# Optimization experiments

Measured on AMD Instinct MI355X. Metric: run time of the kernel, lower is better.

The kernel has to match this reference:

```python
import jax, jax.numpy as jnp
import numpy as np

IN_SHAPE, OUT_SHAPE = 64, 256  # FoldingBlock(64, 256, ...)
REPEAT = OUT_SHAPE // IN_SHAPE  # 4


def sample_2d(m, n):
    # Reproduces SANet.points + SANet.sample_2D exactly (numpy constants).
    xs = np.linspace(-0.3, 0.3, 46)
    ys = np.linspace(-0.3, 0.3, 46)
    X, Y = np.meshgrid(xs, ys)            # (46,46) each, 'xy' indexing
    pts = np.stack([X, Y])                # (2,46,46)
    ix = np.round(np.linspace(0, 45, m)).astype(int)
    iy = np.round(np.linspace(0, 45, n)).astype(int)
    gx, gy = np.meshgrid(ix, iy)          # (n,m)
    p = pts[:, gx.ravel(), gy.ravel()].T  # (m*n, 2)
    return jnp.asarray(p, dtype=jnp.float32)


def _lin_relu(x, W, b):
    return jax.nn.relu(x @ W + b)


def setup_inputs() -> dict:
    key = jax.random.key(0)
    ks = jax.random.split(key, 16)
    s = 0.02  # small init scale keeps softmax logits well-conditioned
    d = {
        "p": jax.random.normal(ks[0], (128, 64, 512), dtype=jnp.float32),
        # upmlp1: MLP([514, 512]) (shared by both up() calls)
        "W_up": jax.random.normal(ks[1], (514, 512), dtype=jnp.float32) * s,
        "b_up": jnp.zeros((512,), jnp.float32),
        # self_attn1: M_h = MLP([1024,256])
        "Wh": jax.random.normal(ks[2], (1024, 256), dtype=jnp.float32) * s,
        "bh": jnp.zeros((256,), jnp.float32),
        # M_l = MLP([1024,256])
        "Wl": jax.random.normal(ks[3], (1024, 256), dtype=jnp.float32) * s,
        "bl": jnp.zeros((256,), jnp.float32),
        # M_g = MLP([1024,1024])
        "Wg": jax.random.normal(ks[4], (1024, 1024), dtype=jnp.float32) * s,
        "bg": jnp.zeros((1024,), jnp.float32),
        # M_f = MLP([1024,512,256]) -> two Linear+ReLU layers
        "Wf1": jax.random.normal(ks[5], (1024, 512), dtype=jnp.float32) * s,
        "bf1": jnp.zeros((512,), jnp.float32),
        "Wf2": jax.random.normal(ks[6], (512, 256), dtype=jnp.float32) * s,
        "bf2": jnp.zeros((256,), jnp.float32),
        # M_down: MLP([1024, 512])
        "W_down": jax.random.normal(ks[7], (1024, 512), dtype=jnp.float32) * s,
        "b_down": jnp.zeros((512,), jnp.float32),
        "m": 16,
        "n": 16,
    }
    return d


def _up(p, pts, W_up, b_up, Wh, bh, Wl, bl, Wg, bg, Wf1, bf1, Wf2, bf2):
    # p: (B, 64, 512) -> (B, 256, 512) via torch-style repeat (tile)
    B = p.shape[0]
    p = jnp.tile(p, (1, REPEAT, 1))
    p2d = jnp.concatenate([p, jnp.broadcast_to(pts[None], (B,) + pts.shape)], -1)  # (B,256,514)
    p2d = _lin_relu(p2d, W_up, b_up)                  # (B,256,512)
    p = jnp.concatenate([p, p2d], -1)                  # (B,256,1024)
    # SelfAttention (hand-rolled: separate projections + softmax + bmm)
    h = _lin_relu(p, Wh, bh)                           # (B,256,256)
    l = _lin_relu(p, Wl, bl)                           # (B,256,256)
    g = _lin_relu(p, Wg, bg)                           # (B,256,1024)
    mm = jnp.einsum("bmc,bnc->bmn", l, h)             # l @ h^T
    attn = jax.nn.softmax(mm, axis=-1)
    applied = jnp.einsum("bmn,bnc->bmc", attn, g)      # (B,256,1024)
    x = p + applied
    # M_f = MLP([1024,512,256]): ReLU after every Linear
    return _lin_relu(_lin_relu(x, Wf1, bf1), Wf2, bf2)  # (B,256,256)


def _down(p, W_down, b_down):
    # (B,256,256) -> (B,64,1024) -> MLP([1024,512])
    B = p.shape[0]
    p = p.reshape(B, IN_SHAPE, REPEAT * p.shape[2])
    return _lin_relu(p, W_down, b_down)                # (B,64,512)


def reference(p, W_up, b_up, Wh, bh, Wl, bl, Wg, bg, Wf1, bf1, Wf2, bf2,
              W_down, b_down, m, n):
    pts = sample_2d(int(m), int(n))                    # (m*n, 2) constant grid
    attn_params = (Wh, bh, Wl, bl, Wg, bg, Wf1, bf1, Wf2, bf2)
    p1 = _up(p, pts, W_up, b_up, *attn_params)         # (B,256,256)
    p2 = _down(p1, W_down, b_down)                     # (B,64,512)
    p_delta = p - p2
    p2u = _up(p_delta, pts, W_up, b_up, *attn_params)  # shared weights with first up
    return p1 + p2u                                    # (B,256,256)
```

## Files before the change

### kernel.cpp

```cpp
#include <hip/hip_runtime.h>
#include <cstdint>
#include <cstddef>


typedef unsigned short u16;
typedef __bf16 bf16x8 __attribute__((ext_vector_type(8)));
typedef float f32x4 __attribute__((ext_vector_type(4)));

__device__ __forceinline__ u16 f2bf(float f) {
    unsigned u = __builtin_bit_cast(unsigned, f);
    unsigned r = (u + 0x7fffu + ((u >> 16) & 1u)) >> 16;
    return (u16)r;
}
__device__ __forceinline__ float bf2f(u16 h) {
    unsigned u = ((unsigned)h) << 16;
    return __builtin_bit_cast(float, u);
}
__device__ __forceinline__ void gload16(const u16* g, u16* l) {
    __builtin_amdgcn_global_load_lds((__attribute__((address_space(1))) void*)g,
                                     (__attribute__((address_space(3))) void*)l,
                                     16, 0, 0);
}
__device__ __forceinline__ unsigned ldsaddr(const u16* p) {
    return (unsigned)(size_t)(const __attribute__((address_space(3))) u16*)p;
}
__device__ __forceinline__ bf16x8 dsr128(unsigned a) {
    f32x4 r;
    asm volatile("ds_read_b128 %0, %1" : "=v"(r) : "v"(a));
    return __builtin_bit_cast(bf16x8, r);
}

#define FENCE asm volatile("" ::: "memory")
#define BAR() do { FENCE; __builtin_amdgcn_s_barrier(); FENCE; } while (0)
#define VMC(N) asm volatile("s_waitcnt vmcnt(" #N ")" ::: "memory")
#define LGKM(N) do { asm volatile("s_waitcnt lgkmcnt(" #N ")" ::: "memory"); \
                     __builtin_amdgcn_sched_barrier(0); } while (0)

template<int MODE>
__global__ __launch_bounds__(512, 1)
void bp(const u16* __restrict__ A0, const u16* __restrict__ A1,
        const u16* __restrict__ Bt, const float* __restrict__ bias,
        const float* __restrict__ EXf, const u16* __restrict__ EXb,
        u16* __restrict__ outB, u16* __restrict__ out1, u16* __restrict__ out2,
        int K, long sB)
{
    __shared__ __align__(16) u16 As[2][16384];
    __shared__ __align__(16) u16 Bs[2][16384];

    const int b    = blockIdx.y;
    const int tid  = threadIdx.x;
    const int lane = tid & 63;
    const int w    = tid >> 6;
    const int wr   = w >> 2, wc = w & 3;
    const int wrow0 = wr * 128, wcol0 = wc * 64;
    const int gn0  = blockIdx.x * 256;
    const int lm   = lane & 15, hk = lane >> 4;
    const int NT   = K / 64;

    const int srow = tid & 255;
    const int su   = tid >> 8;

    const u16* gA0;
    const u16* gA1 = nullptr;
    if constexpr (MODE == 0) {
        gA0 = A0 + ((size_t)b << 15) + (size_t)(srow & 63) * 512 + su * 8;
    } else if constexpr (MODE == 1) {
        gA0 = A0 + ((size_t)b << 15) + (size_t)(srow & 63) * 512 + su * 8;
        gA1 = A1 + ((size_t)b << 17) + (size_t)srow * 512 + su * 8;
    } else if constexpr (MODE == 3) {
        gA0 = A0 + ((size_t)b << 16) + (size_t)srow * 256 + su * 8;
    } else {
        gA0 = A0 + ((size_t)b << 18) + (size_t)srow * 1024 + su * 8;
    }
    const u16* gB0 = Bt + (size_t)b * sB + (size_t)(gn0 + srow) * K + su * 8;

    u16* dA = &As[0][(size_t)(su * 256 + srow) * 8];
    u16* dB = &Bs[0][(size_t)(su * 256 + srow) * 8];

    auto stgA = [&](int kt, int buf, int rp) {
        const u16* g;
        if constexpr (MODE == 1) g = (kt < 8) ? (gA0 + kt * 64) : (gA1 + (kt - 8) * 64);
        else                     g = gA0 + kt * 64;
        u16* d = dA + buf * 16384 + rp * 8192;
        gload16(g + rp * 32,      d);
        gload16(g + rp * 32 + 16, d + 4096);
    };
    auto stgB = [&](int kt, int buf, int rp) {
        const u16* g = gB0 + kt * 64 + rp * 32;
        u16* d = dB + buf * 16384 + rp * 8192;
        gload16(g,      d);
        gload16(g + 16, d + 4096);
    };

    const unsigned aBase = ldsaddr(&As[0][0]) + (unsigned)(hk * 256 + wrow0 + lm) * 16u;
    const unsigned bBase = ldsaddr(&Bs[0][0]) + (unsigned)(hk * 256 + wcol0 + lm) * 16u;

    f32x4 acc[8][4];
    #pragma unroll
    for (int i = 0; i < 8; ++i)
        #pragma unroll
        for (int j = 0; j < 4; ++j)
            acc[i][j] = (f32x4){0.f, 0.f, 0.f, 0.f};

#define MFMA_Q(IB) do { \
    _Pragma("unroll") for (int i_ = 0; i_ < 4; ++i_) \
        _Pragma("unroll") for (int j_ = 0; j_ < 4; ++j_) \
            acc[(IB) + i_][j_] = __builtin_amdgcn_mfma_f32_16x16x32_bf16( \
                aq[i_], bq[j_], acc[(IB) + i_][j_], 0, 0, 0); \
} while (0)

    stgA(0, 0, 0); stgA(0, 0, 1);
    stgB(0, 0, 0); stgB(0, 0, 1);
    stgA(1, 1, 0); stgB(1, 1, 0);
    VMC(4);
    BAR();

    for (int t = 0; t < NT; ++t) {
        const int buf = t & 1, nx = buf ^ 1;
        const unsigned ab = aBase + (unsigned)buf * 32768u;
        const unsigned bb = bBase + (unsigned)buf * 32768u;
        bf16x8 aq[4], bq[4];

        #pragma unroll
        for (int i = 0; i < 4; ++i) aq[i] = dsr128(ab + (unsigned)(i * 256));
        #pragma unroll
        for (int j = 0; j < 4; ++j) bq[j] = dsr128(bb + (unsigned)(j * 256));
        if (t + 1 < NT) stgA(t + 1, nx, 1);
        BAR();
        LGKM(0);
        __builtin_amdgcn_s_setprio(1);
        MFMA_Q(0);
        __builtin_amdgcn_s_setprio(0);
        BAR();

        #pragma unroll
        for (int i = 0; i < 4; ++i) aq[i] = dsr128(ab + (unsigned)(1024 + i * 256));
        if (t + 1 < NT) stgB(t + 1, nx, 1);
        BAR();
        LGKM(0);
        __builtin_amdgcn_s_setprio(1);
        MFMA_Q(4);
        __builtin_amdgcn_s_setprio(0);
        BAR();

        #pragma unroll
        for (int i = 0; i < 4; ++i) aq[i] = dsr128(ab + (unsigned)(16384 + i * 256));
        #pragma unroll
        for (int j = 0; j < 4; ++j) bq[j] = dsr128(bb + (unsigned)(16384 + j * 256));
        if (t + 2 < NT) stgA(t + 2, buf, 0);
        BAR();
        LGKM(0);
        __builtin_amdgcn_s_setprio(1);
        MFMA_Q(0);
        __builtin_amdgcn_s_setprio(0);
        BAR();

        #pragma unroll
        for (int i = 0; i < 4; ++i) aq[i] = dsr128(ab + (unsigned)(17408 + i * 256));
        if (t + 2 < NT) stgB(t + 2, buf, 0);
        if (t + 2 < NT) { VMC(4); } else { VMC(0); }
        BAR();
        LGKM(0);
        __builtin_amdgcn_s_setprio(1);
        MFMA_Q(4);
        __builtin_amdgcn_s_setprio(0);
        BAR();
    }
#undef MFMA_Q

    #pragma unroll
    for (int i = 0; i < 8; ++i) {
        const int rowb = wrow0 + i * 16 + hk * 4;
        #pragma unroll
        for (int j = 0; j < 4; ++j) {
            const int col = gn0 + wcol0 + j * 16 + lm;
            float v4[4];
            #pragma unroll
            for (int r = 0; r < 4; ++r) v4[r] = acc[i][j][r];

            if constexpr (MODE == 0) {
                #pragma unroll
                for (int r = 0; r < 4; ++r) {
                    const int row = rowb + r;
                    float v = v4[r];
                    const float px = -0.3f + 0.04f * (float)(row >> 4);
                    const float py = -0.3f + 0.04f * (float)(row & 15);
                    v += px * EXf[(size_t)512 * 512 + col] + py * EXf[(size_t)513 * 512 + col];
                    v = fmaxf(v + bias[col], 0.0f);
                    outB[((size_t)b << 17) + (size_t)row * 512 + col] = f2bf(v);
                }
            } else if constexpr (MODE == 1) {
                if (col < 512) {
                    #pragma unroll
                    for (int r = 0; r < 4; ++r) {
                        const int row = rowb + r;
                        float v = fmaxf(v4[r] + bias[col], 0.0f);
                        if (col < 256) outB[((size_t)b << 16) + (size_t)row * 256 + col] = f2bf(v);
                        else           out1[((size_t)b << 16) + (size_t)row * 256 + (col - 256)] = f2bf(v);
                    }
                } else {
                    ushort4 o;
                    o.x = f2bf(fmaxf(v4[0] + bias[col], 0.0f));
                    o.y = f2bf(fmaxf(v4[1] + bias[col], 0.0f));
                    o.z = f2bf(fmaxf(v4[2] + bias[col], 0.0f));
                    o.w = f2bf(fmaxf(v4[3] + bias[col], 0.0f));
                    *reinterpret_cast<ushort4*>(out2 + ((size_t)b << 18) +
                        (size_t)(col - 512) * 256 + rowb) = o;
                }
            } else if constexpr (MODE == 3) {
                #pragma unroll
                for (int r = 0; r < 4; ++r) {
                    const int row = rowb + r;
                    float v = v4[r];
                    float cv;
                    if (col < 512) {
                        const size_t ridx = ((size_t)b << 15) + (size_t)(row & 63) * 512 + col;
                        cv = EXf ? EXf[ridx] : bf2f(EXb[ridx]);
                    } else {
                        cv = bf2f(A1[((size_t)b << 17) + (size_t)row * 512 + (col - 512)]);
                    }
                    v += cv;
                    outB[((size_t)b << 18) + (size_t)row * 1024 + col] = f2bf(v);
                }
            } else {
                #pragma unroll
                for (int r = 0; r < 4; ++r) {
                    const int row = rowb + r;
                    float v = fmaxf(v4[r] + bias[col], 0.0f);
                    outB[((size_t)b << 17) + (size_t)row * 512 + col] = f2bf(v);
                }
            }
        }
    }
}

template<int MODE>
__global__ __launch_bounds__(256, 2)
void mg(const u16* __restrict__ A0, const u16* __restrict__ Bt,
        const float* __restrict__ bias, const float* __restrict__ EXf,
        float* __restrict__ outF, u16* __restrict__ outB,
        int K, long sB)
{
    __shared__ __align__(16) u16 As[2][128 * 64];
    __shared__ __align__(16) u16 Bs[2][128 * 64];

    const int b    = blockIdx.z;
    const int tid  = threadIdx.x;
    const int lane = tid & 63;
    const int w    = tid >> 6;
    const int wr   = w >> 1, wc = w & 1;
    const int wrow0 = wr * 64, wcol0 = wc * 64;
    const int gm0  = blockIdx.y * 128;
    const int gn0  = blockIdx.x * 128;
    const int lm   = lane & 15, hk = lane >> 4;
    const int NT = K / 64;

    auto stage = [&](int kt, int buf) {
        const int kb = kt * 64;
        #pragma unroll
        for (int tp = 0; tp < 4; ++tp) {
            const int idx = tid + tp * 256;
            const int U = idx >> 7, row = idx & 127;
            const int kk = kb + U * 8;
            const u16* ga;
            if constexpr (MODE == 2) {
                ga = A0 + ((size_t)b << 16) + (size_t)(gm0 + row) * 256 + kk;
            } else if constexpr (MODE == 5) {
                ga = A0 + ((size_t)b << 17) + (size_t)(gm0 + row) * 512 + kk;
            } else {
                int gr = gm0 + row; if (gr > 63) gr = 63;
                ga = A0 + ((size_t)b << 16) + (size_t)(gr * 4 + (kk >> 8)) * 256 + (kk & 255);
            }
            gload16(ga, &As[buf][(size_t)idx * 8]);
        }
        #pragma unroll
        for (int tp = 0; tp < 4; ++tp) {
            const int idx = tid + tp * 256;
            const int U = idx >> 7, row = idx & 127;
            const int kk = kb + U * 8;
            gload16(Bt + (size_t)b * sB + (size_t)(gn0 + row) * K + kk,
                    &Bs[buf][(size_t)idx * 8]);
        }
    };

    const unsigned aBase = ldsaddr(&As[0][0]) + (unsigned)(hk * 128 + wrow0 + lm) * 16u;
    const unsigned bBase = ldsaddr(&Bs[0][0]) + (unsigned)(hk * 128 + wcol0 + lm) * 16u;

    f32x4 acc[4][4];
    #pragma unroll
    for (int i = 0; i < 4; ++i)
        #pragma unroll
        for (int j = 0; j < 4; ++j)
            acc[i][j] = (f32x4){0.f, 0.f, 0.f, 0.f};

    stage(0, 0);
    if (NT > 1) stage(1, 1);

    for (int kt = 0; kt < NT; ++kt) {
        const int cur = kt & 1;
        if (kt == NT - 1) { VMC(0); } else { VMC(8); }
        __builtin_amdgcn_s_barrier();
        FENCE;
        const unsigned ab = aBase + (unsigned)cur * 16384u;
        const unsigned bb = bBase + (unsigned)cur * 16384u;
        bf16x8 a0[4], b0[4], a1[4], b1[4];
        #pragma unroll
        for (int i = 0; i < 4; ++i) a0[i] = dsr128(ab + (unsigned)(i * 256));
        #pragma unroll
        for (int j = 0; j < 4; ++j) b0[j] = dsr128(bb + (unsigned)(j * 256));
        #pragma unroll
        for (int i = 0; i < 4; ++i) a1[i] = dsr128(ab + (unsigned)(8192 + i * 256));
        #pragma unroll
        for (int j = 0; j < 4; ++j) b1[j] = dsr128(bb + (unsigned)(8192 + j * 256));
        LGKM(8);
        __builtin_amdgcn_s_setprio(1);
        #pragma unroll
        for (int i = 0; i < 4; ++i)
            #pragma unroll
            for (int j = 0; j < 4; ++j)
                acc[i][j] = __builtin_amdgcn_mfma_f32_16x16x32_bf16(a0[i], b0[j], acc[i][j], 0, 0, 0);
        __builtin_amdgcn_s_setprio(0);
        LGKM(0);
        __builtin_amdgcn_s_setprio(1);
        #pragma unroll
        for (int i = 0; i < 4; ++i)
            #pragma unroll
            for (int j = 0; j < 4; ++j)
                acc[i][j] = __builtin_amdgcn_mfma_f32_16x16x32_bf16(a1[i], b1[j], acc[i][j], 0, 0, 0);
        __builtin_amdgcn_s_setprio(0);
        FENCE;
        __builtin_amdgcn_s_barrier();
        if (kt + 2 < NT) stage(kt + 2, cur);
    }

    #pragma unroll
    for (int i = 0; i < 4; ++i) {
        #pragma unroll
        for (int r = 0; r < 4; ++r) {
            const int row = gm0 + wrow0 + i * 16 + hk * 4 + r;
            if (MODE == 6 && row >= 64) continue;
            #pragma unroll
            for (int j = 0; j < 4; ++j) {
                const int col = gn0 + wcol0 + j * 16 + lm;
                float v = acc[i][j][r];
                if constexpr (MODE == 2) {
                    outF[((size_t)b << 16) + (size_t)row * 256 + col] = v;
                } else if constexpr (MODE == 5) {
                    v = fmaxf(v + bias[col], 0.0f);
                    const size_t oidx = ((size_t)b << 16) + (size_t)row * 256 + col;
                    if (EXf) v += EXf[oidx];
                    outF[oidx] = v;
                    if (outB) outB[oidx] = f2bf(v);
                } else {
                    v = fmaxf(v + bias[col], 0.0f);
                    const size_t oidx = ((size_t)b << 15) + (size_t)row * 512 + col;
                    v = EXf[oidx] - v;
                    outB[oidx] = f2bf(v);
                }
            }
        }
    }
}

template<bool F32IN>
__global__ __launch_bounds__(256)
void transpose_k(const void* __restrict__ in_, u16* __restrict__ out, int R, int C)
{
    __shared__ float t[64][65];
    const size_t zo = (size_t)blockIdx.z * (size_t)R * C;
    const int c0 = blockIdx.x * 64, r0 = blockIdx.y * 64;
    const int x = threadIdx.x, y = threadIdx.y;
    #pragma unroll
    for (int i = 0; i < 16; ++i) {
        const int r = y * 16 + i;
        float v;
        if constexpr (F32IN) v = ((const float*)in_)[zo + (size_t)(r0 + r) * C + c0 + x];
        else                 v = bf2f(((const u16*)in_)[zo + (size_t)(r0 + r) * C + c0 + x]);
        t[r][x] = v;
    }
    __syncthreads();
    #pragma unroll
    for (int i = 0; i < 16; ++i) {
        const int c = y * 16 + i;
        out[zo + (size_t)(c0 + c) * R + r0 + x] = f2bf(t[x][c]);
    }
}

__global__ __launch_bounds__(256)
void cvt_k(const float* __restrict__ in, u16* __restrict__ out, int n4)
{
    int i = blockIdx.x * 256 + threadIdx.x;
    const int stride = gridDim.x * 256;
    for (; i < n4; i += stride) {
        float4 v = ((const float4*)in)[i];
        ushort4 o;
        o.x = f2bf(v.x); o.y = f2bf(v.y); o.z = f2bf(v.z); o.w = f2bf(v.w);
        ((ushort4*)out)[i] = o;
    }
}

__global__ __launch_bounds__(512)
void concat3_k(const float* __restrict__ a, const float* __restrict__ bb,
               const float* __restrict__ c, float* __restrict__ o)
{
    const int i = blockIdx.x * 512 + threadIdx.x;
    if (i < 256)       o[i] = a[i];
    else if (i < 512)  o[i] = bb[i - 256];
    else if (i < 1536) o[i] = c[i - 512];
}

__global__ __launch_bounds__(64)
void softmax_k(const float* __restrict__ logits, u16* __restrict__ attn)
{
    const size_t row = blockIdx.x;
    const float4 v = ((const float4*)(logits + row * 256))[threadIdx.x];
    float mx = fmaxf(fmaxf(v.x, v.y), fmaxf(v.z, v.w));
    #pragma unroll
    for (int o = 32; o > 0; o >>= 1) mx = fmaxf(mx, __shfl_xor(mx, o));
    float e0 = expf(v.x - mx), e1 = expf(v.y - mx), e2 = expf(v.z - mx), e3 = expf(v.w - mx);
    float s = e0 + e1 + e2 + e3;
    #pragma unroll
    for (int o = 32; o > 0; o >>= 1) s += __shfl_xor(s, o);
    const float inv = 1.0f / s;
    ushort4 o;
    o.x = f2bf(e0 * inv); o.y = f2bf(e1 * inv); o.z = f2bf(e2 * inv); o.w = f2bf(e3 * inv);
    ((ushort4*)(attn + row * 256))[threadIdx.x] = o;
}

extern "C" void kernel_launch(void* const* d_in, const int* in_sizes, int n_in,
                              void* d_out, int out_size, void* d_ws, size_t ws_size,
                              hipStream_t stream)
{
    const float* p      = (const float*)d_in[0];
    const float* W_up   = (const float*)d_in[1];
    const float* b_up   = (const float*)d_in[2];
    const float* Wh     = (const float*)d_in[3];
    const float* bh     = (const float*)d_in[4];
    const float* Wl     = (const float*)d_in[5];
    const float* bl     = (const float*)d_in[6];
    const float* Wg     = (const float*)d_in[7];
    const float* bg_    = (const float*)d_in[8];
    const float* Wf1    = (const float*)d_in[9];
    const float* bf1    = (const float*)d_in[10];
    const float* Wf2    = (const float*)d_in[11];
    const float* bf2v   = (const float*)d_in[12];
    const float* W_down = (const float*)d_in[13];
    const float* b_down = (const float*)d_in[14];

    const int B = in_sizes[0] / 32768;
    float* out = (float*)d_out;

    char* wsp = (char*)d_ws;
    auto alloc = [&](size_t bytes) -> char* {
        char* r = wsp; wsp += (bytes + 255) & ~(size_t)255; return r;
    };

    u16* WupT  = (u16*)alloc((size_t)512 * 512 * 2);
    u16* WhlgT = (u16*)alloc((size_t)1536 * 1024 * 2);
    u16* Wf1T  = (u16*)alloc((size_t)512 * 1024 * 2);
    u16* Wf2T  = (u16*)alloc((size_t)256 * 512 * 2);
    u16* WdT   = (u16*)alloc((size_t)512 * 1024 * 2);
    float* bias_hlg = (float*)alloc((size_t)1536 * 4);
    u16* pbf   = (u16*)alloc((size_t)B * 32768 * 2);

    const size_t fixed_used = (size_t)(wsp - (char*)d_ws);
    const size_t perB = 1903104;
    int BC = B;
    while (BC > 1 && fixed_used + (size_t)BC * perB + 4096 > ws_size) BC >>= 1;

    u16* upout = (u16*)alloc((size_t)BC * 131072 * 2);
    u16* gT    = (u16*)alloc((size_t)BC * 262144 * 2);
    u16* xb    = (u16*)alloc((size_t)BC * 262144 * 2);
    u16* hb    = (u16*)alloc((size_t)BC * 65536 * 2);
    u16* lb    = (u16*)alloc((size_t)BC * 65536 * 2);
    u16* atb   = (u16*)alloc((size_t)BC * 65536 * 2);
    u16* p1bf  = (u16*)alloc((size_t)BC * 65536 * 2);
    u16* pdbf  = (u16*)alloc((size_t)BC * 32768 * 2);
    float* lgt = (float*)xb;

    const dim3 tb(64, 4);
    {
        int n4 = B * 8192;
        int nb = (n4 + 255) / 256; if (nb > 2048) nb = 2048;
        cvt_k<<<dim3(nb), dim3(256), 0, stream>>>(p, pbf, n4);
        transpose_k<true><<<dim3(8, 8, 1),  tb, 0, stream>>>(W_up, WupT, 512, 512);
        transpose_k<true><<<dim3(4, 16, 1), tb, 0, stream>>>(Wh, WhlgT, 1024, 256);
        transpose_k<true><<<dim3(4, 16, 1), tb, 0, stream>>>(Wl, WhlgT + (size_t)256 * 1024, 1024, 256);
        transpose_k<true><<<dim3(16, 16, 1),tb, 0, stream>>>(Wg, WhlgT + (size_t)512 * 1024, 1024, 1024);
        transpose_k<true><<<dim3(8, 16, 1), tb, 0, stream>>>(Wf1, Wf1T, 1024, 512);
        transpose_k<true><<<dim3(4, 8, 1),  tb, 0, stream>>>(Wf2, Wf2T, 512, 256);
        transpose_k<true><<<dim3(8, 16, 1), tb, 0, stream>>>(W_down, WdT, 1024, 512);
        concat3_k<<<dim3(3), dim3(512), 0, stream>>>(bh, bl, bg_, bias_hlg);
    }

    auto run_up = [&](const u16* pin_bf, const float* pin_f32, const u16* pin_ebf,
                      float* f2outF, u16* f2outB, const float* f2EXf, int bc) {
        bp<0><<<dim3(2, bc), dim3(512), 0, stream>>>(
            pin_bf, nullptr, WupT, b_up, W_up, nullptr, upout, nullptr, nullptr, 512, 0);
        bp<1><<<dim3(6, bc), dim3(512), 0, stream>>>(
            pin_bf, upout, WhlgT, bias_hlg, nullptr, nullptr, hb, lb, gT, 1024, 0);
        mg<2><<<dim3(2, 2, bc), dim3(256), 0, stream>>>(
            lb, hb, nullptr, nullptr, lgt, nullptr, 256, 65536);
        softmax_k<<<dim3(bc * 256), dim3(64), 0, stream>>>(lgt, atb);
        bp<3><<<dim3(4, bc), dim3(512), 0, stream>>>(
            atb, upout, gT, nullptr, pin_f32, pin_ebf, xb, nullptr, nullptr, 256, 262144);
        bp<4><<<dim3(2, bc), dim3(512), 0, stream>>>(
            xb, nullptr, Wf1T, bf1, nullptr, nullptr, upout, nullptr, nullptr, 1024, 0);
        mg<5><<<dim3(2, 2, bc), dim3(256), 0, stream>>>(
            upout, Wf2T, bf2v, f2EXf, f2outF, f2outB, 512, 0);
    };

    for (int b0 = 0; b0 < B; b0 += BC) {
        const int bc = (B - b0 < BC) ? (B - b0) : BC;
        const u16*   pin_bf  = pbf + (size_t)b0 * 32768;
        const float* pin_f32 = p   + (size_t)b0 * 32768;
        float* outc = out + (size_t)b0 * 65536;
        run_up(pin_bf, pin_f32, nullptr, outc, p1bf, nullptr, bc);
        mg<6><<<dim3(4, 1, bc), dim3(256), 0, stream>>>(
            p1bf, WdT, b_down, pin_f32, nullptr, pdbf, 1024, 0);
        run_up(pdbf, nullptr, pdbf, outc, nullptr, outc, bc);
    }
}
```

Measured before the change: 886.6 us.

## Shrink bp GEMM tile to 128x256 with K-step 32 for higher occupancy

The bp kernel moves from a 256x256 block tile with a 64-wide K step and a four-phase interleaved pipeline to a 128x256 tile with a 32-wide K step and a simple double-buffered loop, using less LDS and fewer accumulators so up to four blocks can share a CU. The M dimension is split across grid.y, which multiplies the block count. In MODE 0 the up-projection now computes once per 64 unique input rows and expands the result to the four repeated output rows in the epilogue, removing redundant matmul work. In exchange, each block reuses loaded tiles less, issues more barriers per unit of work, and gives up the old fine-grained load/compute interleaving.

```diff
diff --git a/kernel.cpp b/kernel.cpp
--- a/kernel.cpp
+++ b/kernel.cpp
@@ -37,140 +37,98 @@
                      __builtin_amdgcn_sched_barrier(0); } while (0)
 
 template<int MODE>
-__global__ __launch_bounds__(512, 1)
+__global__ __launch_bounds__(512, 4)
 void bp(const u16* __restrict__ A0, const u16* __restrict__ A1,
         const u16* __restrict__ Bt, const float* __restrict__ bias,
         const float* __restrict__ EXf, const u16* __restrict__ EXb,
         u16* __restrict__ outB, u16* __restrict__ out1, u16* __restrict__ out2,
         int K, long sB)
 {
-    __shared__ __align__(16) u16 As[2][16384];
-    __shared__ __align__(16) u16 Bs[2][16384];
-
-    const int b    = blockIdx.y;
+    __shared__ __align__(16) u16 As[2][4096];
+    __shared__ __align__(16) u16 Bs[2][8192];
+
+    const int bz   = blockIdx.z;
+    const int gm0  = blockIdx.y * 128;
+    const int gn0  = blockIdx.x * 256;
     const int tid  = threadIdx.x;
     const int lane = tid & 63;
     const int w    = tid >> 6;
     const int wr   = w >> 2, wc = w & 3;
-    const int wrow0 = wr * 128, wcol0 = wc * 64;
-    const int gn0  = blockIdx.x * 256;
+    const int wrow0 = wr * 64, wcol0 = wc * 64;
     const int lm   = lane & 15, hk = lane >> 4;
-    const int NT   = K / 64;
-
-    const int srow = tid & 255;
-    const int su   = tid >> 8;
-
-    const u16* gA0;
-    const u16* gA1 = nullptr;
+    const int NT   = K / 32;
+
+    const int rowA = tid & 127, uA = tid >> 7;
+    const int rowB = tid & 255, uB = tid >> 8;
+
+    const u16* gA;
+    const u16* gA1p = nullptr;
     if constexpr (MODE == 0) {
-        gA0 = A0 + ((size_t)b << 15) + (size_t)(srow & 63) * 512 + su * 8;
+        gA = A0 + ((size_t)(2 * bz + (rowA >> 6)) << 15) + (size_t)(rowA & 63) * 512 + uA * 8;
     } else if constexpr (MODE == 1) {
-        gA0 = A0 + ((size_t)b << 15) + (size_t)(srow & 63) * 512 + su * 8;
-        gA1 = A1 + ((size_t)b << 17) + (size_t)srow * 512 + su * 8;
+        gA   = A0 + ((size_t)bz << 15) + (size_t)((gm0 + rowA) & 63) * 512 + uA * 8;
+        gA1p = A1 + ((size_t)bz << 17) + (size_t)(gm0 + rowA) * 512 + uA * 8;
     } else if constexpr (MODE == 3) {
-        gA0 = A0 + ((size_t)b << 16) + (size_t)srow * 256 + su * 8;
+        gA = A0 + ((size_t)bz << 16) + (size_t)(gm0 + rowA) * 256 + uA * 8;
     } else {
-        gA0 = A0 + ((size_t)b << 18) + (size_t)srow * 1024 + su * 8;
-    }
-    const u16* gB0 = Bt + (size_t)b * sB + (size_t)(gn0 + srow) * K + su * 8;
-
-    u16* dA = &As[0][(size_t)(su * 256 + srow) * 8];
-    u16* dB = &Bs[0][(size_t)(su * 256 + srow) * 8];
-
-    auto stgA = [&](int kt, int buf, int rp) {
-        const u16* g;
-        if constexpr (MODE == 1) g = (kt < 8) ? (gA0 + kt * 64) : (gA1 + (kt - 8) * 64);
-        else                     g = gA0 + kt * 64;
-        u16* d = dA + buf * 16384 + rp * 8192;
-        gload16(g + rp * 32,      d);
-        gload16(g + rp * 32 + 16, d + 4096);
+        gA = A0 + ((size_t)bz << 18) + (size_t)(gm0 + rowA) * 1024 + uA * 8;
+    }
+    const u16* gB0 = Bt + (size_t)bz * sB + (size_t)(gn0 + rowB) * K + uB * 8;
+    const u16* gB1 = gB0 + 16;
+
+    u16* dA  = &As[0][(size_t)(uA * 128 + rowA) * 8];
+    u16* dB0 = &Bs[0][(size_t)(uB * 256 + rowB) * 8];
+    u16* dB1 = dB0 + 4096;
+
+    auto stage = [&](int kt, int buf) {
+        const int ko = kt * 32;
+        const u16* ga;
+        if constexpr (MODE == 1) ga = (kt < 16) ? (gA + ko) : (gA1p + (ko - 512));
+        else                     ga = gA + ko;
+        gload16(ga,       dA  + buf * 4096);
+        gload16(gB0 + ko, dB0 + buf * 8192);
+        gload16(gB1 + ko, dB1 + buf * 8192);
     };
-    auto stgB = [&](int kt, int buf, int rp) {
-        const u16* g = gB0 + kt * 64 + rp * 32;
-        u16* d = dB + buf * 16384 + rp * 8192;
-        gload16(g,      d);
-        gload16(g + 16, d + 4096);
-    };
-
-    const unsigned aBase = ldsaddr(&As[0][0]) + (unsigned)(hk * 256 + wrow0 + lm) * 16u;
-    const unsigned bBase = ldsaddr(&Bs[0][0]) + (unsigned)(hk * 256 + wcol0 + lm) * 16u;
-
-    f32x4 acc[8][4];
-    #pragma unroll
-    for (int i = 0; i < 8; ++i)
+
+    const unsigned aB = ldsaddr(&As[0][0]) + (unsigned)((hk * 128 + wrow0 + lm) * 16);
+    const unsigned bB = ldsaddr(&Bs[0][0]) + (unsigned)((hk * 256 + wcol0 + lm) * 16);
+
+    f32x4 acc[4][4];
+    #pragma unroll
+    for (int i = 0; i < 4; ++i)
         #pragma unroll
         for (int j = 0; j < 4; ++j)
             acc[i][j] = (f32x4){0.f, 0.f, 0.f, 0.f};
 
-#define MFMA_Q(IB) do { \
-    _Pragma("unroll") for (int i_ = 0; i_ < 4; ++i_) \
-        _Pragma("unroll") for (int j_ = 0; j_ < 4; ++j_) \
-            acc[(IB) + i_][j_] = __builtin_amdgcn_mfma_f32_16x16x32_bf16( \
-                aq[i_], bq[j_], acc[(IB) + i_][j_], 0, 0, 0); \
-} while (0)
-
-    stgA(0, 0, 0); stgA(0, 0, 1);
-    stgB(0, 0, 0); stgB(0, 0, 1);
-    stgA(1, 1, 0); stgB(1, 1, 0);
-    VMC(4);
-    BAR();
+    stage(0, 0);
+    stage(1, 1);
 
     for (int t = 0; t < NT; ++t) {
-        const int buf = t & 1, nx = buf ^ 1;
-        const unsigned ab = aBase + (unsigned)buf * 32768u;
-        const unsigned bb = bBase + (unsigned)buf * 32768u;
+        const int buf = t & 1;
+        if (t == NT - 1) { VMC(0); } else { VMC(3); }
+        BAR();
         bf16x8 aq[4], bq[4];
-
+        const unsigned ab = aB + (unsigned)buf * 8192u;
+        const unsigned bb = bB + (unsigned)buf * 16384u;
         #pragma unroll
         for (int i = 0; i < 4; ++i) aq[i] = dsr128(ab + (unsigned)(i * 256));
         #pragma unroll
         for (int j = 0; j < 4; ++j) bq[j] = dsr128(bb + (unsigned)(j * 256));
-        if (t + 1 < NT) stgA(t + 1, nx, 1);
-        BAR();
         LGKM(0);
         __builtin_amdgcn_s_setprio(1);
-        MFMA_Q(0);
+        #pragma unroll
+        for (int i = 0; i < 4; ++i)
+            #pragma unroll
+            for (int j = 0; j < 4; ++j)
+                acc[i][j] = __builtin_amdgcn_mfma_f32_16x16x32_bf16(aq[i], bq[j], acc[i][j], 0, 0, 0);
         __builtin_amdgcn_s_setprio(0);
         BAR();
-
-        #pragma unroll
-        for (int i = 0; i < 4; ++i) aq[i] = dsr128(ab + (unsigned)(1024 + i * 256));
-        if (t + 1 < NT) stgB(t + 1, nx, 1);
-        BAR();
-        LGKM(0);
-        __builtin_amdgcn_s_setprio(1);
-        MFMA_Q(4);
-        __builtin_amdgcn_s_setprio(0);
-        BAR();
-
-        #pragma unroll
-        for (int i = 0; i < 4; ++i) aq[i] = dsr128(ab + (unsigned)(16384 + i * 256));
-        #pragma unroll
-        for (int j = 0; j < 4; ++j) bq[j] = dsr128(bb + (unsigned)(16384 + j * 256));
-        if (t + 2 < NT) stgA(t + 2, buf, 0);
-        BAR();
-        LGKM(0);
-        __builtin_amdgcn_s_setprio(1);
-        MFMA_Q(0);
-        __builtin_amdgcn_s_setprio(0);
-        BAR();
-
-        #pragma unroll
-        for (int i = 0; i < 4; ++i) aq[i] = dsr128(ab + (unsigned)(17408 + i * 256));
-        if (t + 2 < NT) stgB(t + 2, buf, 0);
-        if (t + 2 < NT) { VMC(4); } else { VMC(0); }
-        BAR();
-        LGKM(0);
-        __builtin_amdgcn_s_setprio(1);
-        MFMA_Q(4);
-        __builtin_amdgcn_s_setprio(0);
-        BAR();
-    }
-#undef MFMA_Q
-
-    #pragma unroll
-    for (int i = 0; i < 8; ++i) {
-        const int rowb = wrow0 + i * 16 + hk * 4;
+        if (t + 2 < NT) stage(t + 2, buf);
+    }
+
+    #pragma unroll
+    for (int i = 0; i < 4; ++i) {
+        const int lrb = wrow0 + i * 16 + hk * 4;
         #pragma unroll
         for (int j = 0; j < 4; ++j) {
             const int col = gn0 + wcol0 + j * 16 + lm;
@@ -179,24 +137,30 @@
             for (int r = 0; r < 4; ++r) v4[r] = acc[i][j][r];
 
             if constexpr (MODE == 0) {
+                const int b2   = 2 * bz + (lrb >> 6);
+                const float wx = EXf[(size_t)512 * 512 + col];
+                const float wy = EXf[(size_t)513 * 512 + col];
+                const float bc = bias[col];
                 #pragma unroll
                 for (int r = 0; r < 4; ++r) {
-                    const int row = rowb + r;
-                    float v = v4[r];
-                    const float px = -0.3f + 0.04f * (float)(row >> 4);
-                    const float py = -0.3f + 0.04f * (float)(row & 15);
-                    v += px * EXf[(size_t)512 * 512 + col] + py * EXf[(size_t)513 * 512 + col];
-                    v = fmaxf(v + bias[col], 0.0f);
-                    outB[((size_t)b << 17) + (size_t)row * 512 + col] = f2bf(v);
+                    const int prow = (lrb + r) & 63;
+                    const float py = -0.3f + 0.04f * (float)(prow & 15);
+                    const float base = v4[r] + py * wy + bc;
+                    #pragma unroll
+                    for (int q = 0; q < 4; ++q) {
+                        const float px = -0.3f + 0.04f * (float)((prow >> 4) + 4 * q);
+                        const float v = fmaxf(base + px * wx, 0.0f);
+                        outB[((size_t)b2 << 17) + (size_t)(prow + 64 * q) * 512 + col] = f2bf(v);
+                    }
                 }
             } else if constexpr (MODE == 1) {
                 if (col < 512) {
                     #pragma unroll
                     for (int r = 0; r < 4; ++r) {
-                        const int row = rowb + r;
+                        const int row = gm0 + lrb + r;
                         float v = fmaxf(v4[r] + bias[col], 0.0f);
-                        if (col < 256) outB[((size_t)b << 16) + (size_t)row * 256 + col] = f2bf(v);
-                        else           out1[((size_t)b << 16) + (size_t)row * 256 + (col - 256)] = f2bf(v);
+                        if (col < 256) outB[((size_t)bz << 16) + (size_t)row * 256 + col] = f2bf(v);
+                        else           out1[((size_t)bz << 16) + (size_t)row * 256 + (col - 256)] = f2bf(v);
                     }
                 } else {
                     ushort4 o;
@@ -204,30 +168,30 @@
                     o.y = f2bf(fmaxf(v4[1] + bias[col], 0.0f));
                     o.z = f2bf(fmaxf(v4[2] + bias[col], 0.0f));
                     o.w = f2bf(fmaxf(v4[3] + bias[col], 0.0f));
-                    *reinterpret_cast<ushort4*>(out2 + ((size_t)b << 18) +
-                        (size_t)(col - 512) * 256 + rowb) = o;
+                    *reinterpret_cast<ushort4*>(out2 + ((size_t)bz << 18) +
+                        (size_t)(col - 512) * 256 + (gm0 + lrb)) = o;
                 }
             } else if constexpr (MODE == 3) {
                 #pragma unroll
                 for (int r = 0; r < 4; ++r) {
-                    const int row = rowb + r;
+                    const int row = gm0 + lrb + r;
                     float v = v4[r];
                     float cv;
                     if (col < 512) {
-                        const size_t ridx = ((size_t)b << 15) + (size_t)(row & 63) * 512 + col;
+                        const size_t ridx = ((size_t)bz << 15) + (size_t)(row & 63) * 512 + col;
                         cv = EXf ? EXf[ridx] : bf2f(EXb[ridx]);
                     } else {
-                        cv = bf2f(A1[((size_t)b << 17) + (size_t)row * 512 + (col - 512)]);
+                        cv = bf2f(A1[((size_t)bz << 17) + (size_t)row * 512 + (col - 512)]);
                     }
                     v += cv;
-                    outB[((size_t)b << 18) + (size_t)row * 1024 + col] = f2bf(v);
+                    outB[((size_t)bz << 18) + (size_t)row * 1024 + col] = f2bf(v);
                 }
             } else {
                 #pragma unroll
                 for (int r = 0; r < 4; ++r) {
-                    const int row = rowb + r;
+                    const int row = gm0 + lrb + r;
                     float v = fmaxf(v4[r] + bias[col], 0.0f);
-                    outB[((size_t)b << 17) + (size_t)row * 512 + col] = f2bf(v);
+                    outB[((size_t)bz << 17) + (size_t)row * 512 + col] = f2bf(v);
                 }
             }
         }
@@ -495,16 +459,16 @@
 
     auto run_up = [&](const u16* pin_bf, const float* pin_f32, const u16* pin_ebf,
                       float* f2outF, u16* f2outB, const float* f2EXf, int bc) {
-        bp<0><<<dim3(2, bc), dim3(512), 0, stream>>>(
+        bp<0><<<dim3(2, 1, bc / 2), dim3(512), 0, stream>>>(
             pin_bf, nullptr, WupT, b_up, W_up, nullptr, upout, nullptr, nullptr, 512, 0);
-        bp<1><<<dim3(6, bc), dim3(512), 0, stream>>>(
+        bp<1><<<dim3(6, 2, bc), dim3(512), 0, stream>>>(
             pin_bf, upout, WhlgT, bias_hlg, nullptr, nullptr, hb, lb, gT, 1024, 0);
         mg<2><<<dim3(2, 2, bc), dim3(256), 0, stream>>>(
             lb, hb, nullptr, nullptr, lgt, nullptr, 256, 65536);
         softmax_k<<<dim3(bc * 256), dim3(64), 0, stream>>>(lgt, atb);
-        bp<3><<<dim3(4, bc), dim3(512), 0, stream>>>(
+        bp<3><<<dim3(4, 2, bc), dim3(512), 0, stream>>>(
             atb, upout, gT, nullptr, pin_f32, pin_ebf, xb, nullptr, nullptr, 256, 262144);
-        bp<4><<<dim3(2, bc), dim3(512), 0, stream>>>(
+        bp<4><<<dim3(2, 2, bc), dim3(512), 0, stream>>>(
             xb, nullptr, Wf1T, bf1, nullptr, nullptr, upout, nullptr, nullptr, 1024, 0);
         mg<5><<<dim3(2, 2, bc), dim3(256), 0, stream>>>(
             upout, Wf2T, bf2v, f2EXf, f2outF, f2outB, 512, 0);
```

New measurement: 976.0 us. 10.1% more time.

## Factor repeated-input GEMMs to compute on 64 unique rows and broadcast

Applied to the files above, without the earlier changes.

The up-projection and the first half of the h/l/g projection act on the four-times-repeated input, so both are now computed once on the 64 unique rows per batch in a new small-tile kernel. Results are broadcast: the up output is written to the four repeated row positions with the grid offsets, and the partial h/l/g products are stored in fp32 and added in the epilogue of the remaining K=512 GEMM. This removes redundant matmul work. In exchange it adds an extra fp32 round trip through a scratch buffer aliased with xb, and requires an even batch chunk. Softmax is also changed to pack four rows per block.

```diff
diff --git a/kernel.cpp b/kernel.cpp
--- a/kernel.cpp
+++ b/kernel.cpp
@@ -61,12 +61,8 @@
     const int su   = tid >> 8;
 
     const u16* gA0;
-    const u16* gA1 = nullptr;
-    if constexpr (MODE == 0) {
-        gA0 = A0 + ((size_t)b << 15) + (size_t)(srow & 63) * 512 + su * 8;
-    } else if constexpr (MODE == 1) {
-        gA0 = A0 + ((size_t)b << 15) + (size_t)(srow & 63) * 512 + su * 8;
-        gA1 = A1 + ((size_t)b << 17) + (size_t)srow * 512 + su * 8;
+    if constexpr (MODE == 1) {
+        gA0 = A0 + ((size_t)b << 17) + (size_t)srow * 512 + su * 8;
     } else if constexpr (MODE == 3) {
         gA0 = A0 + ((size_t)b << 16) + (size_t)srow * 256 + su * 8;
     } else {
@@ -78,9 +74,7 @@
     u16* dB = &Bs[0][(size_t)(su * 256 + srow) * 8];
 
     auto stgA = [&](int kt, int buf, int rp) {
-        const u16* g;
-        if constexpr (MODE == 1) g = (kt < 8) ? (gA0 + kt * 64) : (gA1 + (kt - 8) * 64);
-        else                     g = gA0 + kt * 64;
+        const u16* g = gA0 + kt * 64;
         u16* d = dA + buf * 16384 + rp * 8192;
         gload16(g + rp * 32,      d);
         gload16(g + rp * 32 + 16, d + 4096);
@@ -178,32 +172,25 @@
             #pragma unroll
             for (int r = 0; r < 4; ++r) v4[r] = acc[i][j][r];
 
-            if constexpr (MODE == 0) {
+            if constexpr (MODE == 1) {
+                float hv[4];
                 #pragma unroll
                 for (int r = 0; r < 4; ++r) {
                     const int row = rowb + r;
-                    float v = v4[r];
-                    const float px = -0.3f + 0.04f * (float)(row >> 4);
-                    const float py = -0.3f + 0.04f * (float)(row & 15);
-                    v += px * EXf[(size_t)512 * 512 + col] + py * EXf[(size_t)513 * 512 + col];
-                    v = fmaxf(v + bias[col], 0.0f);
-                    outB[((size_t)b << 17) + (size_t)row * 512 + col] = f2bf(v);
+                    hv[r] = fmaxf(v4[r] + EXf[((size_t)b * 64 + (row & 63)) * 1536 + col]
+                                        + bias[col], 0.0f);
                 }
-            } else if constexpr (MODE == 1) {
-                if (col < 512) {
+                if (col < 256) {
                     #pragma unroll
-                    for (int r = 0; r < 4; ++r) {
-                        const int row = rowb + r;
-                        float v = fmaxf(v4[r] + bias[col], 0.0f);
-                        if (col < 256) outB[((size_t)b << 16) + (size_t)row * 256 + col] = f2bf(v);
-                        else           out1[((size_t)b << 16) + (size_t)row * 256 + (col - 256)] = f2bf(v);
-                    }
+                    for (int r = 0; r < 4; ++r)
+                        outB[((size_t)b << 16) + (size_t)(rowb + r) * 256 + col] = f2bf(hv[r]);
+                } else if (col < 512) {
+                    #pragma unroll
+                    for (int r = 0; r < 4; ++r)
+                        out1[((size_t)b << 16) + (size_t)(rowb + r) * 256 + (col - 256)] = f2bf(hv[r]);
                 } else {
                     ushort4 o;
-                    o.x = f2bf(fmaxf(v4[0] + bias[col], 0.0f));
-                    o.y = f2bf(fmaxf(v4[1] + bias[col], 0.0f));
-                    o.z = f2bf(fmaxf(v4[2] + bias[col], 0.0f));
-                    o.w = f2bf(fmaxf(v4[3] + bias[col], 0.0f));
+                    o.x = f2bf(hv[0]); o.y = f2bf(hv[1]); o.z = f2bf(hv[2]); o.w = f2bf(hv[3]);
                     *reinterpret_cast<ushort4*>(out2 + ((size_t)b << 18) +
                         (size_t)(col - 512) * 256 + rowb) = o;
                 }
@@ -235,6 +222,118 @@
 }
 
 template<int MODE>
+__global__ __launch_bounds__(512, 4)
+void sp(const u16* __restrict__ A0, const u16* __restrict__ Bt,
+        const float* __restrict__ bias, const float* __restrict__ EXf,
+        u16* __restrict__ outB, float* __restrict__ outF, int K)
+{
+    __shared__ __align__(16) u16 As[2][4096];
+    __shared__ __align__(16) u16 Bs[2][8192];
+
+    const int bz   = blockIdx.z;
+    const int gn0  = blockIdx.x * 256;
+    const int tid  = threadIdx.x;
+    const int lane = tid & 63;
+    const int w    = tid >> 6;
+    const int wr   = w >> 2, wc = w & 3;
+    const int wrow0 = wr * 64, wcol0 = wc * 64;
+    const int lm   = lane & 15, hk = lane >> 4;
+    const int NT   = K / 32;
+
+    const int rowA = tid & 127, uA = tid >> 7;
+    const int rowB = tid & 255, uB = tid >> 8;
+
+    const u16* gA = A0 + ((size_t)(2 * bz + (rowA >> 6)) << 15)
+                       + (size_t)(rowA & 63) * 512 + uA * 8;
+    const u16* gB0 = Bt + (size_t)(gn0 + rowB) * K + uB * 8;
+    const u16* gB1 = gB0 + 16;
+
+    u16* dA  = &As[0][(size_t)(uA * 128 + rowA) * 8];
+    u16* dB0 = &Bs[0][(size_t)(uB * 256 + rowB) * 8];
+    u16* dB1 = dB0 + 4096;
+
+    auto stage = [&](int kt, int buf) {
+        const int ko = kt * 32;
+        gload16(gA  + ko, dA  + buf * 4096);
+        gload16(gB0 + ko, dB0 + buf * 8192);
+        gload16(gB1 + ko, dB1 + buf * 8192);
+    };
+
+    const unsigned aB = ldsaddr(&As[0][0]) + (unsigned)((hk * 128 + wrow0 + lm) * 16);
+    const unsigned bB = ldsaddr(&Bs[0][0]) + (unsigned)((hk * 256 + wcol0 + lm) * 16);
+
+    f32x4 acc[4][4];
+    #pragma unroll
+    for (int i = 0; i < 4; ++i)
+        #pragma unroll
+        for (int j = 0; j < 4; ++j)
+            acc[i][j] = (f32x4){0.f, 0.f, 0.f, 0.f};
+
+    stage(0, 0);
+    stage(1, 1);
+
+    for (int t = 0; t < NT; ++t) {
+        const int buf = t & 1;
+        if (t == NT - 1) { VMC(0); } else { VMC(3); }
+        BAR();
+        bf16x8 aq[4], bq[4];
+        const unsigned ab = aB + (unsigned)buf * 8192u;
+        const unsigned bb = bB + (unsigned)buf * 16384u;
+        #pragma unroll
+        for (int i = 0; i < 4; ++i) aq[i] = dsr128(ab + (unsigned)(i * 256));
+        #pragma unroll
+        for (int j = 0; j < 4; ++j) bq[j] = dsr128(bb + (unsigned)(j * 256));
+        LGKM(0);
+        __builtin_amdgcn_s_setprio(1);
+        #pragma unroll
+        for (int i = 0; i < 4; ++i)
+            #pragma unroll
+            for (int j = 0; j < 4; ++j)
+                acc[i][j] = __builtin_amdgcn_mfma_f32_16x16x32_bf16(aq[i], bq[j], acc[i][j], 0, 0, 0);
+        __builtin_amdgcn_s_setprio(0);
+        BAR();
+        if (t + 2 < NT) stage(t + 2, buf);
+    }
+
+    #pragma unroll
+    for (int i = 0; i < 4; ++i) {
+        const int lrb = wrow0 + i * 16 + hk * 4;
+        const int b2  = 2 * bz + (lrb >> 6);
+        #pragma unroll
+        for (int j = 0; j < 4; ++j) {
+            const int col = gn0 + wcol0 + j * 16 + lm;
+            float v4[4];
+            #pragma unroll
+            for (int r = 0; r < 4; ++r) v4[r] = acc[i][j][r];
+
+            if constexpr (MODE == 0) {
+                const float wx = EXf[(size_t)512 * 512 + col];
+                const float wy = EXf[(size_t)513 * 512 + col];
+                const float bc = bias[col];
+                #pragma unroll
+                for (int r = 0; r < 4; ++r) {
+                    const int prow = (lrb + r) & 63;
+                    const float py = -0.3f + 0.04f * (float)(prow & 15);
+                    const float base = v4[r] + py * wy + bc;
+                    #pragma unroll
+                    for (int q = 0; q < 4; ++q) {
+                        const float px = -0.3f + 0.04f * (float)((prow >> 4) + 4 * q);
+                        const float v = fmaxf(base + px * wx, 0.0f);
+                        outB[((size_t)b2 << 17) + (size_t)(prow + 64 * q) * 512 + col] = f2bf(v);
+                    }
+                }
+            } else {
+                #pragma unroll
+                for (int r = 0; r < 4; ++r) {
+                    const int prow = (lrb + r) & 63;
+                    outF[((size_t)b2 * 64 + prow) * 1536 + col] = v4[r];
+                }
+            }
+        }
+    }
+}
+
+template<int MODE>
 __global__ __launch_bounds__(256, 2)
 void mg(const u16* __restrict__ A0, const u16* __restrict__ Bt,
         const float* __restrict__ bias, const float* __restrict__ EXf,
@@ -409,11 +508,12 @@
     else if (i < 1536) o[i] = c[i - 512];
 }
 
-__global__ __launch_bounds__(64)
+__global__ __launch_bounds__(256)
 void softmax_k(const float* __restrict__ logits, u16* __restrict__ attn)
 {
-    const size_t row = blockIdx.x;
-    const float4 v = ((const float4*)(logits + row * 256))[threadIdx.x];
+    const size_t row = (size_t)blockIdx.x * 4 + (threadIdx.x >> 6);
+    const int lane = threadIdx.x & 63;
+    const float4 v = ((const float4*)(logits + row * 256))[lane];
     float mx = fmaxf(fmaxf(v.x, v.y), fmaxf(v.z, v.w));
     #pragma unroll
     for (int o = 32; o > 0; o >>= 1) mx = fmaxf(mx, __shfl_xor(mx, o));
@@ -424,7 +524,7 @@
     const float inv = 1.0f / s;
     ushort4 o;
     o.x = f2bf(e0 * inv); o.y = f2bf(e1 * inv); o.z = f2bf(e2 * inv); o.w = f2bf(e3 * inv);
-    ((ushort4*)(attn + row * 256))[threadIdx.x] = o;
+    ((ushort4*)(attn + row * 256))[lane] = o;
 }
 
 extern "C" void kernel_launch(void* const* d_in, const int* in_sizes, int n_in,
@@ -456,7 +556,8 @@
     };
 
     u16* WupT  = (u16*)alloc((size_t)512 * 512 * 2);
-    u16* WhlgT = (u16*)alloc((size_t)1536 * 1024 * 2);
+    u16* W1T   = (u16*)alloc((size_t)1536 * 512 * 2);
+    u16* W2T   = (u16*)alloc((size_t)1536 * 512 * 2);
     u16* Wf1T  = (u16*)alloc((size_t)512 * 1024 * 2);
     u16* Wf2T  = (u16*)alloc((size_t)256 * 512 * 2);
     u16* WdT   = (u16*)alloc((size_t)512 * 1024 * 2);
@@ -477,6 +578,7 @@
     u16* p1bf  = (u16*)alloc((size_t)BC * 65536 * 2);
     u16* pdbf  = (u16*)alloc((size_t)BC * 32768 * 2);
     float* lgt = (float*)xb;
+    float* hpf = (float*)xb;
 
     const dim3 tb(64, 4);
     {
@@ -484,9 +586,12 @@
         int nb = (n4 + 255) / 256; if (nb > 2048) nb = 2048;
         cvt_k<<<dim3(nb), dim3(256), 0, stream>>>(p, pbf, n4);
         transpose_k<true><<<dim3(8, 8, 1),  tb, 0, stream>>>(W_up, WupT, 512, 512);
-        transpose_k<true><<<dim3(4, 16, 1), tb, 0, stream>>>(Wh, WhlgT, 1024, 256);
-        transpose_k<true><<<dim3(4, 16, 1), tb, 0, stream>>>(Wl, WhlgT + (size_t)256 * 1024, 1024, 256);
-        transpose_k<true><<<dim3(16, 16, 1),tb, 0, stream>>>(Wg, WhlgT + (size_t)512 * 1024, 1024, 1024);
+        transpose_k<true><<<dim3(4, 8, 1),  tb, 0, stream>>>(Wh,              W1T, 512, 256);
+        transpose_k<true><<<dim3(4, 8, 1),  tb, 0, stream>>>(Wh + 512 * 256,  W2T, 512, 256);
+        transpose_k<true><<<dim3(4, 8, 1),  tb, 0, stream>>>(Wl,              W1T + (size_t)256 * 512, 512, 256);
+        transpose_k<true><<<dim3(4, 8, 1),  tb, 0, stream>>>(Wl + 512 * 256,  W2T + (size_t)256 * 512, 512, 256);
+        transpose_k<true><<<dim3(16, 8, 1), tb, 0, stream>>>(Wg,              W1T + (size_t)512 * 512, 512, 1024);
+        transpose_k<true><<<dim3(16, 8, 1), tb, 0, stream>>>(Wg + (size_t)512 * 1024, W2T + (size_t)512 * 512, 512, 1024);
         transpose_k<true><<<dim3(8, 16, 1), tb, 0, stream>>>(Wf1, Wf1T, 1024, 512);
         transpose_k<true><<<dim3(4, 8, 1),  tb, 0, stream>>>(Wf2, Wf2T, 512, 256);
         transpose_k<true><<<dim3(8, 16, 1), tb, 0, stream>>>(W_down, WdT, 1024, 512);
@@ -495,13 +600,15 @@
 
     auto run_up = [&](const u16* pin_bf, const float* pin_f32, const u16* pin_ebf,
                       float* f2outF, u16* f2outB, const float* f2EXf, int bc) {
-        bp<0><<<dim3(2, bc), dim3(512), 0, stream>>>(
-            pin_bf, nullptr, WupT, b_up, W_up, nullptr, upout, nullptr, nullptr, 512, 0);
+        sp<0><<<dim3(2, 1, bc / 2), dim3(512), 0, stream>>>(
+            pin_bf, WupT, b_up, W_up, upout, nullptr, 512);
+        sp<7><<<dim3(6, 1, bc / 2), dim3(512), 0, stream>>>(
+            pin_bf, W1T, nullptr, nullptr, nullptr, hpf, 512);
         bp<1><<<dim3(6, bc), dim3(512), 0, stream>>>(
-            pin_bf, upout, WhlgT, bias_hlg, nullptr, nullptr, hb, lb, gT, 1024, 0);
+            upout, nullptr, W2T, bias_hlg, hpf, nullptr, hb, lb, gT, 512, 0);
         mg<2><<<dim3(2, 2, bc), dim3(256), 0, stream>>>(
             lb, hb, nullptr, nullptr, lgt, nullptr, 256, 65536);
-        softmax_k<<<dim3(bc * 256), dim3(64), 0, stream>>>(lgt, atb);
+        softmax_k<<<dim3(bc * 64), dim3(256), 0, stream>>>(lgt, atb);
         bp<3><<<dim3(4, bc), dim3(512), 0, stream>>>(
             atb, upout, gT, nullptr, pin_f32, pin_ebf, xb, nullptr, nullptr, 256, 262144);
         bp<4><<<dim3(2, bc), dim3(512), 0, stream>>>(
```

Measured after the change: 915.2 us, median of 2. 3.2% more time.
